# Kernel tuning notes

Hardware: AMD Instinct MI355X
Metric: run time of the kernel (lower is better)

Reference implementation:

```python
import jax, jax.numpy as jnp
import numpy as np

THRESH = 0.3
LENS = 0.4
DECAY = 0.2


@jax.custom_vjp
def act_fun(x):
    return (x > THRESH).astype(x.dtype)

def _act_fwd(x):
    return act_fun(x), x

def _act_bwd(x, g):
    return (g * (jnp.abs(x - THRESH) < LENS).astype(g.dtype),)

act_fun.defvjp(_act_fwd, _act_bwd)


def _conv(x, w):
    # 3x3, stride 1, padding 1, NCHW/OIHW (no bias)
    return jax.lax.conv_general_dilated(
        x, w, (1, 1), ((1, 1), (1, 1)),
        dimension_numbers=("NCHW", "OIHW", "NCHW"))


def _pool2(x):
    # avg_pool2d(k=2) applied per trailing hh-channel: x is (B,C,H,W,4)
    B, C, H, W, K = x.shape
    return x.reshape(B, C, H // 2, 2, W // 2, 2, K).mean(axis=(3, 5))


def _mem_update(x, mem, spike):
    m = mem * DECAY * (1.0 - spike) + x
    return m, act_fun(m)


def _lif_step(drives3, inner, mem, spike):
    # drives3: 3 conv drives (B,C,H,W); inner drives channel 3
    ms, ss = [], []
    for k in range(3):
        m, s = _mem_update(drives3[k], mem[..., k], spike[..., k])
        ms.append(m); ss.append(s)
    m, s = _mem_update(inner, mem[..., 3], spike[..., 3])
    ms.append(m); ss.append(s)
    return jnp.stack(ms, axis=-1), jnp.stack(ss, axis=-1)


def setup_inputs() -> dict:
    key = jax.random.key(0)
    ks = jax.random.split(key, 11)
    B, T = 256, 3
    sc = 0.1
    return {
        "x": jax.random.normal(ks[0], (B, 1, 36, 36), jnp.float32),
        "w1": jax.random.normal(ks[1], (3, 10, 1, 3, 3), jnp.float32) * sc,
        "b1": jax.random.normal(ks[2], (3, 10), jnp.float32) * sc,
        "w2": jax.random.normal(ks[3], (3, 10, 10, 3, 3), jnp.float32) * sc,
        "b2": jax.random.normal(ks[4], (3, 10), jnp.float32) * sc,
        "lif_w": jax.random.normal(ks[5], (1, 3), jnp.float32) * sc,
        "lif_b": jax.random.normal(ks[6], (1,), jnp.float32) * sc,
        "fc_w": jax.random.normal(ks[7], (50, 3240), jnp.float32) * 0.02,
        "fc_b": jax.random.normal(ks[8], (50,), jnp.float32) * sc,
        "task_w": jax.random.normal(ks[9], (T, 10, 50), jnp.float32) * sc,
        "task_b": jax.random.normal(ks[10], (T, 10), jnp.float32) * sc,
        "time_window": 10,
    }


def reference(x, w1, b1, w2, b2, lif_w, lif_b, fc_w, fc_b, task_w, task_b, time_window):
    B = x.shape[0]
    c1_mem = jnp.zeros((B, 10, 36, 36, 4), x.dtype)
    c1_spk = jnp.zeros_like(c1_mem)
    c2_mem = jnp.zeros((B, 10, 18, 18, 4), x.dtype)
    c2_spk = jnp.zeros_like(c2_mem)
    h1 = jnp.zeros((B, 3240), x.dtype)

    # layer-1 drives depend only on the (constant) input: compute once
    drives1 = [_conv(x, w1[k]) + b1[k][:, None, None] for k in range(3)]

    def step(carry, _):
        c1_mem, c1_spk, c2_mem, c2_spk, h1 = carry
        # layer 1 (is_spike_input=False)
        inner1 = jnp.einsum("bchwk,ok->bchwo", c1_mem[..., 0:3], lif_w)[..., 0] + lif_b[0]
        c1_mem_n, c1_spk_n = _lif_step(drives1, inner1, c1_mem, c1_spk)
        p1 = _pool2(c1_spk_n)  # (B,10,18,18,4)
        # layer 2 (is_spike_input=True): sum of conv over 4 slices = conv(sum)+4*bias
        s = p1.sum(axis=-1)
        drives2 = [_conv(s, w2[k]) + 4.0 * b2[k][:, None, None] for k in range(3)]
        inner2 = jnp.einsum("bchwk,ok->bchwo", c2_mem[..., 0:3], lif_w)[..., 0] + lif_b[0]
        c2_mem_n, c2_spk_n = _lif_step(drives2, inner2, c2_mem, c2_spk)
        p2 = _pool2(c2_spk_n)  # (B,10,9,9,4)
        h1 = h1 + p2.reshape(B, -1)
        return (c1_mem_n, c1_spk_n, c2_mem_n, c2_spk_n, h1), None

    carry, _ = jax.lax.scan(step, (c1_mem, c1_spk, c2_mem, c2_spk, h1), None, length=time_window)
    h1 = carry[4]
    outs = (h1 / time_window) @ fc_w.T + fc_b  # (B,50)
    out = jnp.einsum("bf,tof->bto", outs, task_w) + task_b[None]  # (B,T,10)
    return out
```

## Files before the change

### kernel.cpp

```cpp
#include <hip/hip_runtime.h>

#define TH  0.3f
#define DEC 0.2f

#define OFF_X    0
#define OFF_W1   1444
#define OFF_B1   1724
#define OFF_W2   1756
#define OFF_B2   4556
#define OFF_LIF  4588
#define OFF_S    4592
#define OFF_C1X  8592
#define OFF_C2   11448
#define SMEM_N   25218

__device__ __forceinline__ float spikef(float v) { return v > TH ? 1.f : 0.f; }

__device__ __forceinline__ float ag_w(float v) {
    float a;
    asm("v_accvgpr_write_b32 %0, %1" : "=a"(a) : "v"(v));
    return a;
}
__device__ __forceinline__ float ag_r(float a) {
    float v;
    asm("v_accvgpr_read_b32 %0, %1" : "=v"(v) : "a"(a));
    return v;
}

#define AG16_DECL(P) \
    float P##0=ag_w(0.f), P##1=ag_w(0.f), P##2=ag_w(0.f), P##3=ag_w(0.f),   \
          P##4=ag_w(0.f), P##5=ag_w(0.f), P##6=ag_w(0.f), P##7=ag_w(0.f),   \
          P##8=ag_w(0.f), P##9=ag_w(0.f), P##10=ag_w(0.f), P##11=ag_w(0.f), \
          P##12=ag_w(0.f), P##13=ag_w(0.f), P##14=ag_w(0.f), P##15=ag_w(0.f)

#define LIF4(M, D0, D1, D2)                                            \
    {                                                                  \
        float inner_ = fmaf((M).x, lw0, fmaf((M).y, lw1, fmaf((M).z, lw2, lb))); \
        (M).x = ((M).x > TH ? 0.f : (M).x * DEC) + (D0);               \
        (M).y = ((M).y > TH ? 0.f : (M).y * DEC) + (D1);               \
        (M).z = ((M).z > TH ? 0.f : (M).z * DEC) + (D2);               \
        (M).w = ((M).w > TH ? 0.f : (M).w * DEC) + inner_;             \
    }

#define CONV27(WB, ACC)                                                      \
    do {                                                                     \
        float4 w4_;                                                          \
        _Pragma("unroll")                                                    \
        for (int j_ = 0; j_ < 27; ++j_) {                                    \
            if ((j_ & 3) == 0)                                               \
                w4_ = *reinterpret_cast<const float4*>(&sm[(WB) + j_]);      \
            const float wv_ = ((j_ & 3) == 0) ? w4_.x :                      \
                              ((j_ & 3) == 1) ? w4_.y :                      \
                              ((j_ & 3) == 2) ? w4_.z : w4_.w;               \
            const int k_ = j_ / 9, r_ = (j_ - k_ * 9) / 3,                   \
                      c_ = j_ - k_ * 9 - r_ * 3;                             \
            ACC(k_, r_, c_, wv_);                                            \
        }                                                                    \
    } while (0)

#define ACC_L1(K, R, C, W)                                   \
    d[0][K] = fmaf(xv[R][C],         (W), d[0][K]);          \
    d[1][K] = fmaf(xv[R][C + 1],     (W), d[1][K]);          \
    d[2][K] = fmaf(xv[R + 1][C],     (W), d[2][K]);          \
    d[3][K] = fmaf(xv[R + 1][C + 1], (W), d[3][K]);

#define ACC_L2(K, R, C, W)                                   \
    acc[0][K] = fmaf(sv[R][C],         (W), acc[0][K]);      \
    acc[1][K] = fmaf(sv[R][C + 1],     (W), acc[1][K]);      \
    acc[2][K] = fmaf(sv[R + 1][C],     (W), acc[2][K]);      \
    acc[3][K] = fmaf(sv[R + 1][C + 1], (W), acc[3][K]);

__device__ __forceinline__ void conv1(const float* __restrict__ sm, int cell,
                                      float (&d)[4][3])
{
    int oc  = cell / 324;
    int rem = cell - oc * 324;
    int hh  = rem / 18;
    int ww  = rem - hh * 18;
    int y0 = 2 * hh, x0 = 2 * ww;

    float xv[4][4];
#pragma unroll
    for (int r = 0; r < 4; ++r) {
        float2 a = *reinterpret_cast<const float2*>(&sm[OFF_X + (y0 + r) * 38 + x0]);
        float2 b = *reinterpret_cast<const float2*>(&sm[OFF_X + (y0 + r) * 38 + x0 + 2]);
        xv[r][0] = a.x; xv[r][1] = a.y; xv[r][2] = b.x; xv[r][3] = b.y;
    }
    {
        float b0  = sm[OFF_B1 + oc];
        float b1v = sm[OFF_B1 + 10 + oc];
        float b2v = sm[OFF_B1 + 20 + oc];
#pragma unroll
        for (int p = 0; p < 4; ++p) { d[p][0] = b0; d[p][1] = b1v; d[p][2] = b2v; }
    }
    CONV27(OFF_W1 + oc * 28, ACC_L1);
}

__device__ __forceinline__ void conv2(const float* __restrict__ sm, int cell,
                                      float (&acc)[4][3])
{
    int oc  = cell / 81;
    int rem = cell - oc * 81;
    int hh  = rem / 9;
    int ww  = rem - hh * 9;
    int y0 = 2 * hh, x0 = 2 * ww;

    {
        float b20 = 4.f * sm[OFF_B2 + oc];
        float b21 = 4.f * sm[OFF_B2 + 10 + oc];
        float b22 = 4.f * sm[OFF_B2 + 20 + oc];
#pragma unroll
        for (int p = 0; p < 4; ++p) { acc[p][0] = b20; acc[p][1] = b21; acc[p][2] = b22; }
    }

    const int sb = OFF_S + y0 * 20 + x0;
    const int wb = OFF_W2 + (oc * 10) * 28;

    for (int ic = 0; ic < 10; ++ic) {
        float sv[4][4];
#pragma unroll
        for (int r = 0; r < 4; ++r) {
            float2 a = *reinterpret_cast<const float2*>(&sm[sb + ic * 400 + r * 20]);
            float2 b = *reinterpret_cast<const float2*>(&sm[sb + ic * 400 + r * 20 + 2]);
            sv[r][0] = a.x; sv[r][1] = a.y; sv[r][2] = b.x; sv[r][3] = b.y;
        }
        CONV27(wb + ic * 28, ACC_L2);
    }
}

#define L1_AG_CELL(P, CELL)                                                   \
    {                                                                         \
        const int cell_ = (CELL);                                             \
        float d[4][3];                                                        \
        conv1(sm, cell_, d);                                                  \
        float ssum = 0.f; float4 m;                                           \
        m = make_float4(ag_r(P##0), ag_r(P##1), ag_r(P##2), ag_r(P##3));      \
        LIF4(m, d[0][0], d[0][1], d[0][2]);                                   \
        ssum += spikef(m.x) + spikef(m.y) + spikef(m.z) + spikef(m.w);        \
        P##0=ag_w(m.x); P##1=ag_w(m.y); P##2=ag_w(m.z); P##3=ag_w(m.w);       \
        m = make_float4(ag_r(P##4), ag_r(P##5), ag_r(P##6), ag_r(P##7));      \
        LIF4(m, d[1][0], d[1][1], d[1][2]);                                   \
        ssum += spikef(m.x) + spikef(m.y) + spikef(m.z) + spikef(m.w);        \
        P##4=ag_w(m.x); P##5=ag_w(m.y); P##6=ag_w(m.z); P##7=ag_w(m.w);       \
        m = make_float4(ag_r(P##8), ag_r(P##9), ag_r(P##10), ag_r(P##11));    \
        LIF4(m, d[2][0], d[2][1], d[2][2]);                                   \
        ssum += spikef(m.x) + spikef(m.y) + spikef(m.z) + spikef(m.w);        \
        P##8=ag_w(m.x); P##9=ag_w(m.y); P##10=ag_w(m.z); P##11=ag_w(m.w);     \
        m = make_float4(ag_r(P##12), ag_r(P##13), ag_r(P##14), ag_r(P##15));  \
        LIF4(m, d[3][0], d[3][1], d[3][2]);                                   \
        ssum += spikef(m.x) + spikef(m.y) + spikef(m.z) + spikef(m.w);        \
        P##12=ag_w(m.x); P##13=ag_w(m.y); P##14=ag_w(m.z); P##15=ag_w(m.w);   \
        int oc_ = cell_ / 324, rem_ = cell_ - oc_ * 324;                      \
        int hh_ = rem_ / 18, ww_ = rem_ - hh_ * 18;                           \
        sm[OFF_S + oc_ * 400 + (hh_ + 1) * 20 + (ww_ + 1)] = ssum * 0.25f;    \
    }

__attribute__((amdgpu_waves_per_eu(4, 4)))
__global__ __launch_bounds__(1024)
void scnn_kernel(const float* __restrict__ x,
                 const float* __restrict__ w1, const float* __restrict__ b1,
                 const float* __restrict__ w2, const float* __restrict__ b2,
                 const float* __restrict__ lif_w, const float* __restrict__ lif_b,
                 const float* __restrict__ fc_w, const float* __restrict__ fc_b,
                 const float* __restrict__ task_w, const float* __restrict__ task_b,
                 const int* __restrict__ tw_ptr,
                 float* __restrict__ out)
{
    __shared__ float sm[SMEM_N];
    const int tid = threadIdx.x;
    const int b   = blockIdx.x;
    const int T   = tw_ptr[0];

    for (int i = tid; i < SMEM_N; i += 1024) sm[i] = 0.f;
    __syncthreads();

    for (int i = tid; i < 1296; i += 1024) {
        int h = i / 36, w = i - h * 36;
        sm[OFF_X + (h + 1) * 38 + (w + 1)] = x[b * 1296 + i];
    }
    if (tid < 270) {
        int k = tid / 90, r = tid - k * 90;
        int oc = r / 9, j = r - oc * 9;
        sm[OFF_W1 + oc * 28 + k * 9 + j] = w1[tid];
    }
    if (tid < 30)  sm[OFF_B1 + tid] = b1[tid];
    for (int i = tid; i < 2700; i += 1024) {
        int k = i / 900, r1 = i - k * 900;
        int oc = r1 / 90, r2 = r1 - oc * 90;
        int ic = r2 / 9,  j  = r2 - ic * 9;
        sm[OFF_W2 + (oc * 10 + ic) * 28 + k * 9 + j] = w2[i];
    }
    if (tid < 30)  sm[OFF_B2 + tid] = b2[tid];
    if (tid < 3)   sm[OFF_LIF + tid] = lif_w[tid];
    if (tid == 0)  sm[OFF_LIF + 3] = lif_b[0];
    __syncthreads();

    const float lw0 = sm[OFF_LIF + 0], lw1 = sm[OFF_LIF + 1],
                lw2 = sm[OFF_LIF + 2], lb  = sm[OFF_LIF + 3];

    AG16_DECL(aA);
    AG16_DECL(aB);
    AG16_DECL(aC);
    float hA0=0.f,hA1=0.f,hA2=0.f,hA3=0.f;

    for (int t = 0; t < T; ++t) {
        L1_AG_CELL(aA, tid);
        __builtin_amdgcn_sched_barrier(0);
        L1_AG_CELL(aB, tid + 1024);
        __builtin_amdgcn_sched_barrier(0);
        L1_AG_CELL(aC, tid + 2048);
        __builtin_amdgcn_sched_barrier(0);
        if (tid < 3240 - 3072) {
            const int cell = tid + 3072;
            float d[4][3];
            conv1(sm, cell, d);
            float* cp = &sm[OFF_C1X + tid * 17];
            float ssum = 0.f;
#pragma unroll
            for (int p = 0; p < 4; ++p) {
                float4 m = make_float4(cp[4*p], cp[4*p+1], cp[4*p+2], cp[4*p+3]);
                LIF4(m, d[p][0], d[p][1], d[p][2]);
                ssum += spikef(m.x) + spikef(m.y) + spikef(m.z) + spikef(m.w);
                cp[4*p] = m.x; cp[4*p+1] = m.y; cp[4*p+2] = m.z; cp[4*p+3] = m.w;
            }
            int oc_ = cell / 324, rem_ = cell - oc_ * 324;
            int hh_ = rem_ / 18, ww_ = rem_ - hh_ * 18;
            sm[OFF_S + oc_ * 400 + (hh_ + 1) * 20 + (ww_ + 1)] = ssum * 0.25f;
        }
        __syncthreads();

        if (tid < 810) {
            float acc[4][3];
            conv2(sm, tid, acc);
            float* cp = &sm[OFF_C2 + tid * 17];
#pragma unroll
            for (int p = 0; p < 4; ++p) {
                float4 m = make_float4(cp[4*p], cp[4*p+1], cp[4*p+2], cp[4*p+3]);
                LIF4(m, acc[p][0], acc[p][1], acc[p][2]);
                hA0 += spikef(m.x) * 0.25f; hA1 += spikef(m.y) * 0.25f;
                hA2 += spikef(m.z) * 0.25f; hA3 += spikef(m.w) * 0.25f;
                cp[4*p] = m.x; cp[4*p+1] = m.y; cp[4*p+2] = m.z; cp[4*p+3] = m.w;
            }
        }
        __syncthreads();
    }

    if (tid < 810)
        *reinterpret_cast<float4*>(&sm[OFF_S + tid * 4]) = make_float4(hA0, hA1, hA2, hA3);
    __syncthreads();

    float invT = 1.f / (float)T;
    int f = tid >> 4, g = tid & 15;
    if (f < 50) {
        const float* wrow = fc_w + f * 3240;
        float p0 = 0.f, p1 = 0.f;
        for (int j = g; j + 16 < 3240; j += 32) {
            p0 = fmaf(sm[OFF_S + j], wrow[j], p0);
            p1 = fmaf(sm[OFF_S + j + 16], wrow[j + 16], p1);
        }
        { int j = 3232 + g; if (j < 3240) p0 = fmaf(sm[OFF_S + j], wrow[j], p0); }
        float p = p0 + p1;
        p += __shfl_xor(p, 1);
        p += __shfl_xor(p, 2);
        p += __shfl_xor(p, 4);
        p += __shfl_xor(p, 8);
        if (g == 0) sm[OFF_X + f] = p * invT + fc_b[f];
    }
    __syncthreads();

    if (tid < 30) {
        float acc = task_b[tid];
        const float* twp = task_w + tid * 50;
        for (int j = 0; j < 50; ++j) acc = fmaf(sm[OFF_X + j], twp[j], acc);
        out[b * 30 + tid] = acc;
    }
}

extern "C" void kernel_launch(void* const* d_in, const int* in_sizes, int n_in,
                              void* d_out, int out_size, void* d_ws, size_t ws_size,
                              hipStream_t stream) {
    const float* x      = (const float*)d_in[0];
    const float* w1     = (const float*)d_in[1];
    const float* b1     = (const float*)d_in[2];
    const float* w2     = (const float*)d_in[3];
    const float* b2     = (const float*)d_in[4];
    const float* lif_w  = (const float*)d_in[5];
    const float* lif_b  = (const float*)d_in[6];
    const float* fc_w   = (const float*)d_in[7];
    const float* fc_b   = (const float*)d_in[8];
    const float* task_w = (const float*)d_in[9];
    const float* task_b = (const float*)d_in[10];
    const int*   tw     = (const int*)d_in[11];

    int B = in_sizes[0] / 1296;

    scnn_kernel<<<B, 1024, 0, stream>>>(x, w1, b1, w2, b2, lif_w, lif_b,
                                        fc_w, fc_b, task_w, task_b, tw,
                                        (float*)d_out);
}
```

Measured before the change: 212.0 us.

## Move conv weights to global workspace and layer-2 membrane state into AGPRs

Conv1 and conv2 weights are no longer staged in LDS. They are written to a global workspace and read from there, relying on cache. The layer-2 membrane state moves from LDS into a fourth bank of accumulation registers. Together these shrink shared memory from about 25K to 8K floats, likely to allow more blocks per CU. The risks are that every block writes the shared workspace concurrently with no grid-level synchronisation before reading it, and that weight reads now go through the global cache path instead of LDS.

```diff
diff --git a/kernel.cpp b/kernel.cpp
--- a/kernel.cpp
+++ b/kernel.cpp
@@ -4,15 +4,12 @@
 #define DEC 0.2f
 
 #define OFF_X    0
-#define OFF_W1   1444
-#define OFF_B1   1724
-#define OFF_W2   1756
-#define OFF_B2   4556
-#define OFF_LIF  4588
-#define OFF_S    4592
-#define OFF_C1X  8592
-#define OFF_C2   11448
-#define SMEM_N   25218
+#define OFF_B1   1444
+#define OFF_B2   1476
+#define OFF_LIF  1508
+#define OFF_S    1512
+#define OFF_C1X  5512
+#define SMEM_N   8368
 
 __device__ __forceinline__ float spikef(float v) { return v > TH ? 1.f : 0.f; }
 
@@ -42,13 +39,13 @@
         (M).w = ((M).w > TH ? 0.f : (M).w * DEC) + inner_;             \
     }
 
-#define CONV27(WB, ACC)                                                      \
+#define CONV27(WP, ACC)                                                      \
     do {                                                                     \
         float4 w4_;                                                          \
         _Pragma("unroll")                                                    \
         for (int j_ = 0; j_ < 27; ++j_) {                                    \
             if ((j_ & 3) == 0)                                               \
-                w4_ = *reinterpret_cast<const float4*>(&sm[(WB) + j_]);      \
+                w4_ = *reinterpret_cast<const float4*>((WP) + j_);           \
             const float wv_ = ((j_ & 3) == 0) ? w4_.x :                      \
                               ((j_ & 3) == 1) ? w4_.y :                      \
                               ((j_ & 3) == 2) ? w4_.z : w4_.w;               \
@@ -70,7 +67,8 @@
     acc[2][K] = fmaf(sv[R + 1][C],     (W), acc[2][K]);      \
     acc[3][K] = fmaf(sv[R + 1][C + 1], (W), acc[3][K]);
 
-__device__ __forceinline__ void conv1(const float* __restrict__ sm, int cell,
+__device__ __forceinline__ void conv1(const float* __restrict__ sm,
+                                      const float* __restrict__ w1r, int cell,
                                       float (&d)[4][3])
 {
     int oc  = cell / 324;
@@ -93,10 +91,11 @@
 #pragma unroll
         for (int p = 0; p < 4; ++p) { d[p][0] = b0; d[p][1] = b1v; d[p][2] = b2v; }
     }
-    CONV27(OFF_W1 + oc * 28, ACC_L1);
-}
-
-__device__ __forceinline__ void conv2(const float* __restrict__ sm, int cell,
+    CONV27(w1r + oc * 28, ACC_L1);
+}
+
+__device__ __forceinline__ void conv2(const float* __restrict__ sm,
+                                      const float* __restrict__ w2r, int cell,
                                       float (&acc)[4][3])
 {
     int oc  = cell / 81;
@@ -114,7 +113,7 @@
     }
 
     const int sb = OFF_S + y0 * 20 + x0;
-    const int wb = OFF_W2 + (oc * 10) * 28;
+    const float* wb = w2r + (oc * 10) * 28;
 
     for (int ic = 0; ic < 10; ++ic) {
         float sv[4][4];
@@ -132,7 +131,7 @@
     {                                                                         \
         const int cell_ = (CELL);                                             \
         float d[4][3];                                                        \
-        conv1(sm, cell_, d);                                                  \
+        conv1(sm, w1r, cell_, d);                                             \
         float ssum = 0.f; float4 m;                                           \
         m = make_float4(ag_r(P##0), ag_r(P##1), ag_r(P##2), ag_r(P##3));      \
         LIF4(m, d[0][0], d[0][1], d[0][2]);                                   \
@@ -164,13 +163,16 @@
                  const float* __restrict__ fc_w, const float* __restrict__ fc_b,
                  const float* __restrict__ task_w, const float* __restrict__ task_b,
                  const int* __restrict__ tw_ptr,
-                 float* __restrict__ out)
+                 float* __restrict__ out, float* __restrict__ wsf)
 {
     __shared__ float sm[SMEM_N];
     const int tid = threadIdx.x;
     const int b   = blockIdx.x;
     const int T   = tw_ptr[0];
 
+    const float* w1r = wsf;
+    const float* w2r = wsf + 512;
+
     for (int i = tid; i < SMEM_N; i += 1024) sm[i] = 0.f;
     __syncthreads();
 
@@ -181,14 +183,14 @@
     if (tid < 270) {
         int k = tid / 90, r = tid - k * 90;
         int oc = r / 9, j = r - oc * 9;
-        sm[OFF_W1 + oc * 28 + k * 9 + j] = w1[tid];
+        wsf[oc * 28 + k * 9 + j] = w1[tid];
     }
     if (tid < 30)  sm[OFF_B1 + tid] = b1[tid];
     for (int i = tid; i < 2700; i += 1024) {
         int k = i / 900, r1 = i - k * 900;
         int oc = r1 / 90, r2 = r1 - oc * 90;
         int ic = r2 / 9,  j  = r2 - ic * 9;
-        sm[OFF_W2 + (oc * 10 + ic) * 28 + k * 9 + j] = w2[i];
+        wsf[512 + (oc * 10 + ic) * 28 + k * 9 + j] = w2[i];
     }
     if (tid < 30)  sm[OFF_B2 + tid] = b2[tid];
     if (tid < 3)   sm[OFF_LIF + tid] = lif_w[tid];
@@ -201,6 +203,7 @@
     AG16_DECL(aA);
     AG16_DECL(aB);
     AG16_DECL(aC);
+    AG16_DECL(aP);
     float hA0=0.f,hA1=0.f,hA2=0.f,hA3=0.f;
 
     for (int t = 0; t < T; ++t) {
@@ -213,7 +216,7 @@
         if (tid < 3240 - 3072) {
             const int cell = tid + 3072;
             float d[4][3];
-            conv1(sm, cell, d);
+            conv1(sm, w1r, cell, d);
             float* cp = &sm[OFF_C1X + tid * 17];
             float ssum = 0.f;
 #pragma unroll
@@ -231,16 +234,28 @@
 
         if (tid < 810) {
             float acc[4][3];
-            conv2(sm, tid, acc);
-            float* cp = &sm[OFF_C2 + tid * 17];
-#pragma unroll
-            for (int p = 0; p < 4; ++p) {
-                float4 m = make_float4(cp[4*p], cp[4*p+1], cp[4*p+2], cp[4*p+3]);
-                LIF4(m, acc[p][0], acc[p][1], acc[p][2]);
-                hA0 += spikef(m.x) * 0.25f; hA1 += spikef(m.y) * 0.25f;
-                hA2 += spikef(m.z) * 0.25f; hA3 += spikef(m.w) * 0.25f;
-                cp[4*p] = m.x; cp[4*p+1] = m.y; cp[4*p+2] = m.z; cp[4*p+3] = m.w;
-            }
+            conv2(sm, w2r, tid, acc);
+            float4 m;
+            m = make_float4(ag_r(aP0), ag_r(aP1), ag_r(aP2), ag_r(aP3));
+            LIF4(m, acc[0][0], acc[0][1], acc[0][2]);
+            hA0 += spikef(m.x) * 0.25f; hA1 += spikef(m.y) * 0.25f;
+            hA2 += spikef(m.z) * 0.25f; hA3 += spikef(m.w) * 0.25f;
+            aP0=ag_w(m.x); aP1=ag_w(m.y); aP2=ag_w(m.z); aP3=ag_w(m.w);
+            m = make_float4(ag_r(aP4), ag_r(aP5), ag_r(aP6), ag_r(aP7));
+            LIF4(m, acc[1][0], acc[1][1], acc[1][2]);
+            hA0 += spikef(m.x) * 0.25f; hA1 += spikef(m.y) * 0.25f;
+            hA2 += spikef(m.z) * 0.25f; hA3 += spikef(m.w) * 0.25f;
+            aP4=ag_w(m.x); aP5=ag_w(m.y); aP6=ag_w(m.z); aP7=ag_w(m.w);
+            m = make_float4(ag_r(aP8), ag_r(aP9), ag_r(aP10), ag_r(aP11));
+            LIF4(m, acc[2][0], acc[2][1], acc[2][2]);
+            hA0 += spikef(m.x) * 0.25f; hA1 += spikef(m.y) * 0.25f;
+            hA2 += spikef(m.z) * 0.25f; hA3 += spikef(m.w) * 0.25f;
+            aP8=ag_w(m.x); aP9=ag_w(m.y); aP10=ag_w(m.z); aP11=ag_w(m.w);
+            m = make_float4(ag_r(aP12), ag_r(aP13), ag_r(aP14), ag_r(aP15));
+            LIF4(m, acc[3][0], acc[3][1], acc[3][2]);
+            hA0 += spikef(m.x) * 0.25f; hA1 += spikef(m.y) * 0.25f;
+            hA2 += spikef(m.z) * 0.25f; hA3 += spikef(m.w) * 0.25f;
+            aP12=ag_w(m.x); aP13=ag_w(m.y); aP14=ag_w(m.z); aP15=ag_w(m.w);
         }
         __syncthreads();
     }
@@ -296,5 +311,5 @@
 
     scnn_kernel<<<B, 1024, 0, stream>>>(x, w1, b1, w2, b2, lif_w, lif_b,
                                         fc_w, fc_b, task_w, task_b, tw,
-                                        (float*)d_out);
-}
+                                        (float*)d_out, (float*)d_ws);
+}
```

After: 236.7 us. 11.7% more time.
